# Performance work log

Measured on AMD Instinct MI355X. Metric: run time of the kernel, lower is better.

The kernel has to match this reference:

```python
import jax, jax.numpy as jnp
import numpy as np

INPUT_SIZE = 1024
HIDDEN = [2048, 2048]
OUTPUT_SIZE = 10
N = 16384
PRIOR_VAR = 100.0


def setup_inputs() -> dict:
    key = jax.random.key(0)
    ks = jax.random.split(key, 8)
    X = jax.random.normal(ks[0], (N, INPUT_SIZE), dtype=jnp.float32)
    Y = jax.random.randint(ks[1], (N,), 0, OUTPUT_SIZE, dtype=jnp.int32)
    # Kaiming-ish init like nn.Linear defaults (scale irrelevant to correctness)
    def lin(k, fan_in, fan_out):
        bound = 1.0 / np.sqrt(fan_in)
        kw, kb = jax.random.split(k)
        W = jax.random.uniform(kw, (fan_out, fan_in), jnp.float32, -bound, bound)
        b = jax.random.uniform(kb, (fan_out,), jnp.float32, -bound, bound)
        return W, b
    W1, b1 = lin(ks[2], INPUT_SIZE, HIDDEN[0])
    W2, b2 = lin(ks[3], HIDDEN[0], HIDDEN[1])
    W3, b3 = lin(ks[4], HIDDEN[1], OUTPUT_SIZE)
    return {"X": X, "Y": Y, "W1": W1, "b1": b1, "W2": W2, "b2": b2, "W3": W3, "b3": b3}


def reference(X, Y, W1, b1, W2, b2, W3, b3):
    # Batched version of the per-sample Linear+ReLU+...+Linear+Softmax(dim=0) loop.
    h = jax.nn.relu(X @ W1.T + b1)            # [N, H0]
    h = jax.nn.relu(h @ W2.T + b2)            # [N, H1]
    logits = h @ W3.T + b3                    # [N, C]
    # Categorical(probs=softmax(logits)).log_prob(Y[i]) == log_softmax(logits)[i, Y[i]]
    logp = jax.nn.log_softmax(logits, axis=-1)
    log_likelihood = jnp.sum(jnp.take_along_axis(logp, Y[:, None].astype(jnp.int32), axis=-1))
    # MVN(0, 100*I) log-prob over flattened params: closed-form diagonal Gaussian.
    params = (W1, b1, W2, b2, W3, b3)
    d = sum(p.size for p in params)
    sq = sum(jnp.sum(p * p) for p in params)
    log_prior = -0.5 * (sq / PRIOR_VAR + d * jnp.log(2.0 * jnp.pi * PRIOR_VAR))
    return log_likelihood + log_prior
```

## Files before the change

kernel.cpp:

```cpp
#include <hip/hip_runtime.h>
#include <math.h>

typedef __bf16 bf16;
typedef bf16 bf16x8 __attribute__((ext_vector_type(8)));
typedef bf16 bf16x4 __attribute__((ext_vector_type(4)));
typedef float f32x4 __attribute__((ext_vector_type(4)));

#define NROWS 16384
#define HID 2048

__global__ __launch_bounds__(256) void cvt_kernel(const float* __restrict__ src,
                                                  bf16* __restrict__ dst, int n4) {
  int stride = gridDim.x * blockDim.x;
  for (int i = blockIdx.x * blockDim.x + threadIdx.x; i < n4; i += stride) {
    float4 v = ((const float4*)src)[i];
    bf16x4 o;
    o[0] = (bf16)v.x; o[1] = (bf16)v.y; o[2] = (bf16)v.z; o[3] = (bf16)v.w;
    ((bf16x4*)dst)[i] = o;
  }
}

__device__ __forceinline__ void gload_lds16(const bf16* g, bf16* l) {
  __builtin_amdgcn_global_load_lds((const __attribute__((address_space(1))) void*)g,
                                   (__attribute__((address_space(3))) void*)l,
                                   16, 0, 0);
}

template <int K, bool RELU>
__global__ __launch_bounds__(512) void gemm256(const bf16* __restrict__ A,
                                               const bf16* __restrict__ B,
                                               const float* __restrict__ bias,
                                               bf16* __restrict__ C, int N) {
  extern __shared__ bf16 smem[];
  constexpr int NT = K / 32;
  const int tid = threadIdx.x;
  const int lane = tid & 63;
  const int w = tid >> 6;
  const int wr = w >> 2, wc = w & 3;

  const int c = blockIdx.x & 7, l = blockIdx.x >> 3;
  const int bm = c * 8 + (l >> 3);
  const int bn = l & 7;

  const bf16* Abase = A + (size_t)bm * 256 * K;
  const bf16* Bbase = B + (size_t)bn * 256 * K;

  const int r0 = tid >> 2;
  const int r1 = r0 + 128;
  const int kp = tid & 3;
  const size_t offS0 = (size_t)r0 * K + ((kp ^ ((r0 >> 1) & 3)) * 8);
  const size_t offS1 = (size_t)r1 * K + ((kp ^ ((r1 >> 1) & 3)) * 8);

  int offRA[8], offRB[4];
  const int kk = lane >> 4;
#pragma unroll
  for (int mi = 0; mi < 8; ++mi) {
    const int r = wr * 128 + mi * 16 + (lane & 15);
    offRA[mi] = (r * 4 + (kk ^ ((r >> 1) & 3))) * 8;
  }
#pragma unroll
  for (int ni = 0; ni < 4; ++ni) {
    const int r = wc * 64 + ni * 16 + (lane & 15);
    offRB[ni] = (r * 4 + (kk ^ ((r >> 1) & 3))) * 8 + 8192;
  }

  f32x4 acc[8][4] = {};

#define STAGE(t, b)                                                   \
  {                                                                   \
    const bf16* As = Abase + (size_t)(t) * 32;                        \
    const bf16* Bs = Bbase + (size_t)(t) * 32;                        \
    bf16* d = smem + (b) * 16384 + w * 512;    \
    gload_lds16(As + offS0, d);                                       \
    gload_lds16(As + offS1, d + 4096);                                \
    gload_lds16(Bs + offS0, d + 8192);                                \
    gload_lds16(Bs + offS1, d + 12288);                               \
  }

  STAGE(0, 0); STAGE(1, 1); STAGE(2, 2);
  asm volatile("s_waitcnt vmcnt(8)" ::: "memory");
  __builtin_amdgcn_s_barrier();
  asm volatile("" ::: "memory");

  for (int t = 0; t < NT; ++t) {
    if (t + 3 < NT) STAGE(t + 3, (t + 3) & 3);

    const bf16* base = smem + (t & 3) * 16384;
    bf16x8 af[8], bfr[4];
#pragma unroll
    for (int mi = 0; mi < 8; ++mi) af[mi] = *(const bf16x8*)(base + offRA[mi]);
#pragma unroll
    for (int ni = 0; ni < 4; ++ni) bfr[ni] = *(const bf16x8*)(base + offRB[ni]);

    __builtin_amdgcn_s_setprio(1);
#pragma unroll
    for (int mi = 0; mi < 8; ++mi)
#pragma unroll
      for (int ni = 0; ni < 4; ++ni)
        acc[mi][ni] = __builtin_amdgcn_mfma_f32_16x16x32_bf16(af[mi], bfr[ni], acc[mi][ni], 0, 0, 0);
    __builtin_amdgcn_s_setprio(0);
    asm volatile("" ::: "memory");

    if (t + 1 < NT) {
      if (t + 3 < NT)      asm volatile("s_waitcnt vmcnt(8)" ::: "memory");
      else if (t + 2 < NT) asm volatile("s_waitcnt vmcnt(4)" ::: "memory");
      else                 asm volatile("s_waitcnt vmcnt(0)" ::: "memory");
      __builtin_amdgcn_s_barrier();
      asm volatile("" ::: "memory");
    }
  }
#undef STAGE

  const int crow0 = bm * 256 + wr * 128 + (lane >> 4) * 4;
  const int ccol0 = bn * 256 + wc * 64 + (lane & 15);
#pragma unroll
  for (int mi = 0; mi < 8; ++mi) {
#pragma unroll
    for (int ni = 0; ni < 4; ++ni) {
      const int col = ccol0 + ni * 16;
      const float bv = bias[col];
#pragma unroll
      for (int j = 0; j < 4; ++j) {
        const int row = crow0 + mi * 16 + j;
        float v = acc[mi][ni][j] + bv;
        if (RELU) v = fmaxf(v, 0.f);
        C[(size_t)row * N + col] = (bf16)v;
      }
    }
  }
}

__global__ __launch_bounds__(256) void loss_kernel(const bf16* __restrict__ h2,
                                                   const bf16* __restrict__ W3b,
                                                   const float* __restrict__ b3,
                                                   const int* __restrict__ Y,
                                                   float* __restrict__ acc) {
  __shared__ bf16 w3s[10 * HID];
  for (int i = threadIdx.x; i < 10 * HID / 8; i += 256)
    ((bf16x8*)w3s)[i] = ((const bf16x8*)W3b)[i];
  __syncthreads();

  const int lane = threadIdx.x & 63;
  const int w = threadIdx.x >> 6;
  const int nwave = gridDim.x * 4;
  float lsum = 0.f;

  for (int row = blockIdx.x * 4 + w; row < NROWS; row += nwave) {
    float p[10];
#pragma unroll
    for (int c = 0; c < 10; ++c) p[c] = 0.f;
    const bf16* hrow = h2 + (size_t)row * HID;
#pragma unroll
    for (int it = 0; it < 4; ++it) {
      const int k = it * 512 + lane * 8;
      bf16x8 hv = *(const bf16x8*)&hrow[k];
      float hf[8];
#pragma unroll
      for (int j = 0; j < 8; ++j) hf[j] = (float)hv[j];
#pragma unroll
      for (int c = 0; c < 10; ++c) {
        bf16x8 wv = *(const bf16x8*)&w3s[c * HID + k];
        float dp = 0.f;
#pragma unroll
        for (int j = 0; j < 8; ++j) dp += hf[j] * (float)wv[j];
        p[c] += dp;
      }
    }
#pragma unroll
    for (int off = 32; off; off >>= 1)
#pragma unroll
      for (int c = 0; c < 10; ++c) p[c] += __shfl_xor(p[c], off, 64);

    float lg[10], m = -1e30f;
#pragma unroll
    for (int c = 0; c < 10; ++c) { lg[c] = p[c] + b3[c]; m = fmaxf(m, lg[c]); }
    float s = 0.f;
#pragma unroll
    for (int c = 0; c < 10; ++c) s += expf(lg[c] - m);
    const float lse = m + logf(s);
    const int y = Y[row];
    float ly = 0.f;
#pragma unroll
    for (int c = 0; c < 10; ++c) ly += (c == y) ? lg[c] : 0.f;
    lsum += ly - lse;
  }
  if (lane == 0) atomicAdd(&acc[0], lsum);
}

struct SqArgs { const float* p[6]; int n[6]; };

__global__ __launch_bounds__(256) void sumsq_kernel(SqArgs args, float* __restrict__ acc) {
  float s = 0.f;
  const int stride = gridDim.x * blockDim.x;
  for (int a = 0; a < 6; ++a) {
    const float* p = args.p[a];
    const int n = args.n[a];
    for (int i = blockIdx.x * blockDim.x + threadIdx.x; i < n; i += stride) {
      float v = p[i];
      s += v * v;
    }
  }
#pragma unroll
  for (int off = 32; off; off >>= 1) s += __shfl_xor(s, off, 64);
  if ((threadIdx.x & 63) == 0) atomicAdd(&acc[1], s);
}

__global__ void finalize_kernel(float* __restrict__ out, const float* __restrict__ acc,
                                double dterm) {
  out[0] = (float)((double)acc[0] - 0.5 * ((double)acc[1] / 100.0 + dterm));
}

extern "C" void kernel_launch(void* const* d_in, const int* in_sizes, int n_in,
                              void* d_out, int out_size, void* d_ws, size_t ws_size,
                              hipStream_t stream) {
  const float* X  = (const float*)d_in[0];
  const int*   Y  = (const int*)d_in[1];
  const float* W1 = (const float*)d_in[2];
  const float* b1 = (const float*)d_in[3];
  const float* W2 = (const float*)d_in[4];
  const float* b2 = (const float*)d_in[5];
  const float* W3 = (const float*)d_in[6];
  const float* b3 = (const float*)d_in[7];
  float* out = (float*)d_out;

  char* ws = (char*)d_ws;
  size_t off = 0;
  auto alloc = [&](size_t bytes) -> void* {
    void* p = ws + off;
    off += (bytes + 255) & ~(size_t)255;
    return p;
  };
  bf16* Xb  = (bf16*)alloc((size_t)NROWS * 1024 * 2);
  bf16* W1b = (bf16*)alloc((size_t)HID * 1024 * 2);
  bf16* W2b = (bf16*)alloc((size_t)HID * HID * 2);
  bf16* W3b = (bf16*)alloc((size_t)10 * HID * 2);
  bf16* h1  = (bf16*)alloc((size_t)NROWS * HID * 2);
  bf16* h2  = (bf16*)alloc((size_t)NROWS * HID * 2);
  float* acc = (float*)alloc(256);

  hipMemsetAsync(acc, 0, 16, stream);

  auto cvt = [&](const float* s, bf16* d, int n) {
    int n4 = n / 4;
    int grid = (n4 + 255) / 256;
    if (grid > 4096) grid = 4096;
    cvt_kernel<<<grid, 256, 0, stream>>>(s, d, n4);
  };
  cvt(X,  Xb,  NROWS * 1024);
  cvt(W1, W1b, HID * 1024);
  cvt(W2, W2b, HID * HID);
  cvt(W3, W3b, 10 * HID);

  SqArgs sq;
  sq.p[0] = W1; sq.n[0] = in_sizes[2];
  sq.p[1] = b1; sq.n[1] = in_sizes[3];
  sq.p[2] = W2; sq.n[2] = in_sizes[4];
  sq.p[3] = b2; sq.n[3] = in_sizes[5];
  sq.p[4] = W3; sq.n[4] = in_sizes[6];
  sq.p[5] = b3; sq.n[5] = in_sizes[7];
  sumsq_kernel<<<512, 256, 0, stream>>>(sq, acc);

  hipFuncSetAttribute((const void*)gemm256<1024, true>,
                      hipFuncAttributeMaxDynamicSharedMemorySize, 131072);
  hipFuncSetAttribute((const void*)gemm256<2048, true>,
                      hipFuncAttributeMaxDynamicSharedMemorySize, 131072);

  gemm256<1024, true><<<512, 512, 131072, stream>>>(Xb, W1b, b1, h1, HID);
  gemm256<2048, true><<<512, 512, 131072, stream>>>(h1, W2b, b2, h2, HID);

  loss_kernel<<<256, 256, 0, stream>>>(h2, W3b, b3, Y, acc);

  long long d = 0;
  for (int i = 2; i < 8; ++i) d += in_sizes[i];
  double dterm = (double)d * log(2.0 * M_PI * 100.0);
  finalize_kernel<<<1, 1, 0, stream>>>(out, acc, dterm);
}
```

Measured before the change: 436.7 us.

## Restructure GEMM to 64-wide K double-buffer pipeline and fuse conversion with sum-of-squares

The GEMM now loads 64-wide K tiles into two 64KB LDS buffers with an 8-slot XOR swizzle. Global-to-LDS staging of the next tile is interleaved in half-tile pieces between MFMA groups, separated by barriers. The four conversion kernels and the sumsq kernel are merged into one pass that converts to bf16 and accumulates squares, with b3 squares moved into finalize. The loss kernel grid grows from 256 to 1024 blocks. The many extra barriers per tile and the launch_bounds(512,2) register cap may cost throughput or cause spills.

```diff
diff --git a/kernel.cpp b/kernel.cpp
--- a/kernel.cpp
+++ b/kernel.cpp
@@ -9,107 +9,145 @@
 #define NROWS 16384
 #define HID 2048
 
-__global__ __launch_bounds__(256) void cvt_kernel(const float* __restrict__ src,
-                                                  bf16* __restrict__ dst, int n4) {
-  int stride = gridDim.x * blockDim.x;
-  for (int i = blockIdx.x * blockDim.x + threadIdx.x; i < n4; i += stride) {
-    float4 v = ((const float4*)src)[i];
-    bf16x4 o;
-    o[0] = (bf16)v.x; o[1] = (bf16)v.y; o[2] = (bf16)v.z; o[3] = (bf16)v.w;
-    ((bf16x4*)dst)[i] = o;
-  }
-}
-
 __device__ __forceinline__ void gload_lds16(const bf16* g, bf16* l) {
   __builtin_amdgcn_global_load_lds((const __attribute__((address_space(1))) void*)g,
                                    (__attribute__((address_space(3))) void*)l,
                                    16, 0, 0);
 }
 
+#define MF(a, b, c) __builtin_amdgcn_mfma_f32_16x16x32_bf16((a), (b), (c), 0, 0, 0)
+
+#define BAR()                                  \
+  asm volatile("" ::: "memory");               \
+  __builtin_amdgcn_s_barrier();                \
+  asm volatile("" ::: "memory");
+
 template <int K, bool RELU>
-__global__ __launch_bounds__(512) void gemm256(const bf16* __restrict__ A,
-                                               const bf16* __restrict__ B,
-                                               const float* __restrict__ bias,
-                                               bf16* __restrict__ C, int N) {
+__global__ __launch_bounds__(512, 2) void gemm256(const bf16* __restrict__ A,
+                                                  const bf16* __restrict__ B,
+                                                  const float* __restrict__ bias,
+                                                  bf16* __restrict__ C, int N) {
   extern __shared__ bf16 smem[];
-  constexpr int NT = K / 32;
+  constexpr int NT = K / 64;
+  constexpr int NI = NT / 2;
   const int tid = threadIdx.x;
   const int lane = tid & 63;
   const int w = tid >> 6;
   const int wr = w >> 2, wc = w & 3;
 
-  const int c = blockIdx.x & 7, l = blockIdx.x >> 3;
-  const int bm = c * 8 + (l >> 3);
-  const int bn = l & 7;
+  const int xc = blockIdx.x & 7, xl = blockIdx.x >> 3;
+  const int bm = xc * 8 + (xl >> 3);
+  const int bn = xl & 7;
 
   const bf16* Abase = A + (size_t)bm * 256 * K;
   const bf16* Bbase = B + (size_t)bn * 256 * K;
 
-  const int r0 = tid >> 2;
-  const int r1 = r0 + 128;
-  const int kp = tid & 3;
-  const size_t offS0 = (size_t)r0 * K + ((kp ^ ((r0 >> 1) & 3)) * 8);
-  const size_t offS1 = (size_t)r1 * K + ((kp ^ ((r1 >> 1) & 3)) * 8);
-
-  int offRA[8], offRB[4];
-  const int kk = lane >> 4;
-#pragma unroll
-  for (int mi = 0; mi < 8; ++mi) {
-    const int r = wr * 128 + mi * 16 + (lane & 15);
-    offRA[mi] = (r * 4 + (kk ^ ((r >> 1) & 3))) * 8;
-  }
-#pragma unroll
-  for (int ni = 0; ni < 4; ++ni) {
-    const int r = wc * 64 + ni * 16 + (lane & 15);
-    offRB[ni] = (r * 4 + (kk ^ ((r >> 1) & 3))) * 8 + 8192;
-  }
+  const int srow = tid >> 3;
+  const int sslot = (tid & 7) ^ (srow & 7);
+
+  const int q0 = (lane >> 4) ^ (lane & 7);
+  const int q1 = q0 ^ 4;
+  int rbA[8], rbB[4];
+#pragma unroll
+  for (int mi = 0; mi < 8; ++mi)
+    rbA[mi] = (wr * 128 + mi * 16 + (lane & 15)) * 64;
+#pragma unroll
+  for (int ni = 0; ni < 4; ++ni)
+    rbB[ni] = 16384 + (wc * 64 + ni * 16 + (lane & 15)) * 64;
 
   f32x4 acc[8][4] = {};
-
-#define STAGE(t, b)                                                   \
-  {                                                                   \
-    const bf16* As = Abase + (size_t)(t) * 32;                        \
-    const bf16* Bs = Bbase + (size_t)(t) * 32;                        \
-    bf16* d = smem + (b) * 16384 + w * 512;    \
-    gload_lds16(As + offS0, d);                                       \
-    gload_lds16(As + offS1, d + 4096);                                \
-    gload_lds16(Bs + offS0, d + 8192);                                \
-    gload_lds16(Bs + offS1, d + 12288);                               \
-  }
-
-  STAGE(0, 0); STAGE(1, 1); STAGE(2, 2);
-  asm volatile("s_waitcnt vmcnt(8)" ::: "memory");
-  __builtin_amdgcn_s_barrier();
-  asm volatile("" ::: "memory");
-
-  for (int t = 0; t < NT; ++t) {
-    if (t + 3 < NT) STAGE(t + 3, (t + 3) & 3);
-
-    const bf16* base = smem + (t & 3) * 16384;
-    bf16x8 af[8], bfr[4];
-#pragma unroll
-    for (int mi = 0; mi < 8; ++mi) af[mi] = *(const bf16x8*)(base + offRA[mi]);
-#pragma unroll
-    for (int ni = 0; ni < 4; ++ni) bfr[ni] = *(const bf16x8*)(base + offRB[ni]);
-
-    __builtin_amdgcn_s_setprio(1);
-#pragma unroll
-    for (int mi = 0; mi < 8; ++mi)
-#pragma unroll
-      for (int ni = 0; ni < 4; ++ni)
-        acc[mi][ni] = __builtin_amdgcn_mfma_f32_16x16x32_bf16(af[mi], bfr[ni], acc[mi][ni], 0, 0, 0);
-    __builtin_amdgcn_s_setprio(0);
-    asm volatile("" ::: "memory");
-
-    if (t + 1 < NT) {
-      if (t + 3 < NT)      asm volatile("s_waitcnt vmcnt(8)" ::: "memory");
-      else if (t + 2 < NT) asm volatile("s_waitcnt vmcnt(4)" ::: "memory");
-      else                 asm volatile("s_waitcnt vmcnt(0)" ::: "memory");
-      __builtin_amdgcn_s_barrier();
-      asm volatile("" ::: "memory");
+  bf16x8 av[4], bv[4];
+
+#define LD8(off) (*(const bf16x8*)(smem + (off)))
+
+#define READS_A(bb, qk, mh)                                  \
+  av[0] = LD8((bb)*32768 + rbA[(mh)*4 + 0] + (qk)*8);        \
+  av[1] = LD8((bb)*32768 + rbA[(mh)*4 + 1] + (qk)*8);        \
+  av[2] = LD8((bb)*32768 + rbA[(mh)*4 + 2] + (qk)*8);        \
+  av[3] = LD8((bb)*32768 + rbA[(mh)*4 + 3] + (qk)*8);
+
+#define READS_B(bb, qk)                                      \
+  bv[0] = LD8((bb)*32768 + rbB[0] + (qk)*8);                 \
+  bv[1] = LD8((bb)*32768 + rbB[1] + (qk)*8);                 \
+  bv[2] = LD8((bb)*32768 + rbB[2] + (qk)*8);                 \
+  bv[3] = LD8((bb)*32768 + rbB[3] + (qk)*8);
+
+#define MFMA16(mh)                                           \
+  __builtin_amdgcn_s_setprio(1);                             \
+  acc[(mh)*4+0][0] = MF(av[0], bv[0], acc[(mh)*4+0][0]);     \
+  acc[(mh)*4+0][1] = MF(av[0], bv[1], acc[(mh)*4+0][1]);     \
+  acc[(mh)*4+0][2] = MF(av[0], bv[2], acc[(mh)*4+0][2]);     \
+  acc[(mh)*4+0][3] = MF(av[0], bv[3], acc[(mh)*4+0][3]);     \
+  acc[(mh)*4+1][0] = MF(av[1], bv[0], acc[(mh)*4+1][0]);     \
+  acc[(mh)*4+1][1] = MF(av[1], bv[1], acc[(mh)*4+1][1]);     \
+  acc[(mh)*4+1][2] = MF(av[1], bv[2], acc[(mh)*4+1][2]);     \
+  acc[(mh)*4+1][3] = MF(av[1], bv[3], acc[(mh)*4+1][3]);     \
+  acc[(mh)*4+2][0] = MF(av[2], bv[0], acc[(mh)*4+2][0]);     \
+  acc[(mh)*4+2][1] = MF(av[2], bv[1], acc[(mh)*4+2][1]);     \
+  acc[(mh)*4+2][2] = MF(av[2], bv[2], acc[(mh)*4+2][2]);     \
+  acc[(mh)*4+2][3] = MF(av[2], bv[3], acc[(mh)*4+2][3]);     \
+  acc[(mh)*4+3][0] = MF(av[3], bv[0], acc[(mh)*4+3][0]);     \
+  acc[(mh)*4+3][1] = MF(av[3], bv[1], acc[(mh)*4+3][1]);     \
+  acc[(mh)*4+3][2] = MF(av[3], bv[2], acc[(mh)*4+3][2]);     \
+  acc[(mh)*4+3][3] = MF(av[3], bv[3], acc[(mh)*4+3][3]);     \
+  __builtin_amdgcn_s_setprio(0);
+
+#define STAGE_HALF(isB, h, t, bb)                                                  \
+  {                                                                                \
+    const bf16* gs = ((isB) ? Bbase : Abase) + (size_t)((h)*128) * K + (t) * 64;   \
+    bf16* ld = smem + (bb)*32768 + (isB)*16384 + (h)*8192 + w * 512;               \
+    gload_lds16(gs + (size_t)srow * K + sslot * 8, ld);                            \
+    gload_lds16(gs + (size_t)(srow + 64) * K + sslot * 8, ld + 4096);              \
+  }
+
+  STAGE_HALF(0, 0, 0, 0); STAGE_HALF(0, 1, 0, 0);
+  STAGE_HALF(1, 0, 0, 0); STAGE_HALF(1, 1, 0, 0);
+
+  for (int it = 0; it < NI; ++it) {
+    const int T = 2 * it;
+    const bool s47 = (it < NI - 1);
+
+    STAGE_HALF(0, 0, T + 1, 1);
+    asm volatile("s_waitcnt vmcnt(2)" ::: "memory");
+    BAR();
+    READS_B(0, q0); READS_A(0, q0, 0);
+    MFMA16(0);
+    BAR();
+    READS_A(0, q0, 1);
+    STAGE_HALF(0, 1, T + 1, 1);
+    MFMA16(1);
+    BAR();
+    READS_B(0, q1); READS_A(0, q1, 0);
+    STAGE_HALF(1, 0, T + 1, 1);
+    MFMA16(0);
+    BAR();
+    READS_A(0, q1, 1);
+    STAGE_HALF(1, 1, T + 1, 1);
+    MFMA16(1);
+    BAR();
+    if (s47) {
+      STAGE_HALF(0, 0, T + 2, 0);
+      asm volatile("s_waitcnt vmcnt(2)" ::: "memory");
+    } else {
+      asm volatile("s_waitcnt vmcnt(0)" ::: "memory");
     }
-  }
-#undef STAGE
+    BAR();
+    READS_B(1, q0); READS_A(1, q0, 0);
+    MFMA16(0);
+    BAR();
+    READS_A(1, q0, 1);
+    if (s47) STAGE_HALF(0, 1, T + 2, 0);
+    MFMA16(1);
+    BAR();
+    READS_B(1, q1); READS_A(1, q1, 0);
+    if (s47) STAGE_HALF(1, 0, T + 2, 0);
+    MFMA16(0);
+    BAR();
+    READS_A(1, q1, 1);
+    if (s47) STAGE_HALF(1, 1, T + 2, 0);
+    MFMA16(1);
+    BAR();
+  }
 
   const int crow0 = bm * 256 + wr * 128 + (lane >> 4) * 4;
   const int ccol0 = bn * 256 + wc * 64 + (lane & 15);
@@ -118,16 +156,47 @@
 #pragma unroll
     for (int ni = 0; ni < 4; ++ni) {
       const int col = ccol0 + ni * 16;
-      const float bv = bias[col];
+      const float bvv = bias[col];
 #pragma unroll
       for (int j = 0; j < 4; ++j) {
         const int row = crow0 + mi * 16 + j;
-        float v = acc[mi][ni][j] + bv;
+        float v = acc[mi][ni][j] + bvv;
         if (RELU) v = fmaxf(v, 0.f);
         C[(size_t)row * N + col] = (bf16)v;
       }
     }
   }
+}
+
+struct CvtSqArgs {
+  const float* src[6];
+  bf16* dst[6];
+  int n4[6];
+  int dosq[6];
+};
+
+__global__ __launch_bounds__(256) void cvtsq_kernel(CvtSqArgs a, float* __restrict__ acc) {
+  float s = 0.f;
+  const int stride = gridDim.x * blockDim.x;
+#pragma unroll 1
+  for (int seg = 0; seg < 6; ++seg) {
+    const float4* src = (const float4*)a.src[seg];
+    bf16x4* dst = (bf16x4*)a.dst[seg];
+    const int n4 = a.n4[seg];
+    const bool dq = a.dosq[seg] != 0;
+    for (int i = blockIdx.x * blockDim.x + threadIdx.x; i < n4; i += stride) {
+      float4 v = src[i];
+      if (dst) {
+        bf16x4 o;
+        o[0] = (bf16)v.x; o[1] = (bf16)v.y; o[2] = (bf16)v.z; o[3] = (bf16)v.w;
+        dst[i] = o;
+      }
+      if (dq) s += v.x * v.x + v.y * v.y + v.z * v.z + v.w * v.w;
+    }
+  }
+#pragma unroll
+  for (int off = 32; off; off >>= 1) s += __shfl_xor(s, off, 64);
+  if ((threadIdx.x & 63) == 0) atomicAdd(&acc[1], s);
 }
 
 __global__ __launch_bounds__(256) void loss_kernel(const bf16* __restrict__ h2,
@@ -187,27 +256,11 @@
   if (lane == 0) atomicAdd(&acc[0], lsum);
 }
 
-struct SqArgs { const float* p[6]; int n[6]; };
-
-__global__ __launch_bounds__(256) void sumsq_kernel(SqArgs args, float* __restrict__ acc) {
-  float s = 0.f;
-  const int stride = gridDim.x * blockDim.x;
-  for (int a = 0; a < 6; ++a) {
-    const float* p = args.p[a];
-    const int n = args.n[a];
-    for (int i = blockIdx.x * blockDim.x + threadIdx.x; i < n; i += stride) {
-      float v = p[i];
-      s += v * v;
-    }
-  }
-#pragma unroll
-  for (int off = 32; off; off >>= 1) s += __shfl_xor(s, off, 64);
-  if ((threadIdx.x & 63) == 0) atomicAdd(&acc[1], s);
-}
-
 __global__ void finalize_kernel(float* __restrict__ out, const float* __restrict__ acc,
-                                double dterm) {
-  out[0] = (float)((double)acc[0] - 0.5 * ((double)acc[1] / 100.0 + dterm));
+                                const float* __restrict__ b3, double dterm) {
+  double sq = (double)acc[1];
+  for (int i = 0; i < 10; ++i) sq += (double)b3[i] * (double)b3[i];
+  out[0] = (float)((double)acc[0] - 0.5 * (sq / 100.0 + dterm));
 }
 
 extern "C" void kernel_launch(void* const* d_in, const int* in_sizes, int n_in,
@@ -240,25 +293,14 @@
 
   hipMemsetAsync(acc, 0, 16, stream);
 
-  auto cvt = [&](const float* s, bf16* d, int n) {
-    int n4 = n / 4;
-    int grid = (n4 + 255) / 256;
-    if (grid > 4096) grid = 4096;
-    cvt_kernel<<<grid, 256, 0, stream>>>(s, d, n4);
-  };
-  cvt(X,  Xb,  NROWS * 1024);
-  cvt(W1, W1b, HID * 1024);
-  cvt(W2, W2b, HID * HID);
-  cvt(W3, W3b, 10 * HID);
-
-  SqArgs sq;
-  sq.p[0] = W1; sq.n[0] = in_sizes[2];
-  sq.p[1] = b1; sq.n[1] = in_sizes[3];
-  sq.p[2] = W2; sq.n[2] = in_sizes[4];
-  sq.p[3] = b2; sq.n[3] = in_sizes[5];
-  sq.p[4] = W3; sq.n[4] = in_sizes[6];
-  sq.p[5] = b3; sq.n[5] = in_sizes[7];
-  sumsq_kernel<<<512, 256, 0, stream>>>(sq, acc);
+  CvtSqArgs ca;
+  ca.src[0] = X;  ca.dst[0] = Xb;  ca.n4[0] = NROWS * 1024 / 4; ca.dosq[0] = 0;
+  ca.src[1] = W1; ca.dst[1] = W1b; ca.n4[1] = HID * 1024 / 4;   ca.dosq[1] = 1;
+  ca.src[2] = W2; ca.dst[2] = W2b; ca.n4[2] = HID * HID / 4;    ca.dosq[2] = 1;
+  ca.src[3] = W3; ca.dst[3] = W3b; ca.n4[3] = 10 * HID / 4;     ca.dosq[3] = 1;
+  ca.src[4] = b1; ca.dst[4] = nullptr; ca.n4[4] = HID / 4;      ca.dosq[4] = 1;
+  ca.src[5] = b2; ca.dst[5] = nullptr; ca.n4[5] = HID / 4;      ca.dosq[5] = 1;
+  cvtsq_kernel<<<2048, 256, 0, stream>>>(ca, acc);
 
   hipFuncSetAttribute((const void*)gemm256<1024, true>,
                       hipFuncAttributeMaxDynamicSharedMemorySize, 131072);
@@ -268,10 +310,10 @@
   gemm256<1024, true><<<512, 512, 131072, stream>>>(Xb, W1b, b1, h1, HID);
   gemm256<2048, true><<<512, 512, 131072, stream>>>(h1, W2b, b2, h2, HID);
 
-  loss_kernel<<<256, 256, 0, stream>>>(h2, W3b, b3, Y, acc);
+  loss_kernel<<<1024, 256, 0, stream>>>(h2, W3b, b3, Y, acc);
 
   long long d = 0;
   for (int i = 2; i < 8; ++i) d += in_sizes[i];
   double dterm = (double)d * log(2.0 * M_PI * 100.0);
-  finalize_kernel<<<1, 1, 0, stream>>>(out, acc, dterm);
-}
+  finalize_kernel<<<1, 1, 0, stream>>>(out, acc, b3, dterm);
+}
```

Result: slower. 493.5 us (+13.0%).

## Software-pipeline GEMM LDS fragment loads, fuse convert with sum-of-squares, widen loss grid

Applied to the files above, without the earlier changes.

The GEMM inner loop now processes two K-tiles per iteration and splits A fragments into halves. The next half's LDS reads are issued while the current 16 MFMAs run, so shared-memory latency overlaps with matrix math. The kernel also gets a two-block-per-CU launch bound hint. The four conversion kernels and the sum-of-squares kernel are merged into one pass that reads each weight once, with the b3 squares moved to finalize. The loss kernel grid grows from 256 to 1024 blocks. Together these add register pressure and more complex wait-count logic.

```diff
diff --git a/kernel.cpp b/kernel.cpp
--- a/kernel.cpp
+++ b/kernel.cpp
@@ -9,28 +9,28 @@
 #define NROWS 16384
 #define HID 2048
 
-__global__ __launch_bounds__(256) void cvt_kernel(const float* __restrict__ src,
-                                                  bf16* __restrict__ dst, int n4) {
-  int stride = gridDim.x * blockDim.x;
-  for (int i = blockIdx.x * blockDim.x + threadIdx.x; i < n4; i += stride) {
-    float4 v = ((const float4*)src)[i];
-    bf16x4 o;
-    o[0] = (bf16)v.x; o[1] = (bf16)v.y; o[2] = (bf16)v.z; o[3] = (bf16)v.w;
-    ((bf16x4*)dst)[i] = o;
-  }
-}
-
 __device__ __forceinline__ void gload_lds16(const bf16* g, bf16* l) {
   __builtin_amdgcn_global_load_lds((const __attribute__((address_space(1))) void*)g,
                                    (__attribute__((address_space(3))) void*)l,
                                    16, 0, 0);
 }
 
+#define MF(a, b, c) __builtin_amdgcn_mfma_f32_16x16x32_bf16((a), (b), (c), 0, 0, 0)
+
+#define BAR()                                  \
+  asm volatile("" ::: "memory");               \
+  __builtin_amdgcn_s_barrier();                \
+  asm volatile("" ::: "memory");
+
+#define LGKM0()                                           \
+  asm volatile("s_waitcnt lgkmcnt(0)" ::: "memory");      \
+  __builtin_amdgcn_sched_barrier(0);
+
 template <int K, bool RELU>
-__global__ __launch_bounds__(512) void gemm256(const bf16* __restrict__ A,
-                                               const bf16* __restrict__ B,
-                                               const float* __restrict__ bias,
-                                               bf16* __restrict__ C, int N) {
+__global__ __launch_bounds__(512, 2) void gemm256(const bf16* __restrict__ A,
+                                                  const bf16* __restrict__ B,
+                                                  const float* __restrict__ bias,
+                                                  bf16* __restrict__ C, int N) {
   extern __shared__ bf16 smem[];
   constexpr int NT = K / 32;
   const int tid = threadIdx.x;
@@ -38,9 +38,9 @@
   const int w = tid >> 6;
   const int wr = w >> 2, wc = w & 3;
 
-  const int c = blockIdx.x & 7, l = blockIdx.x >> 3;
-  const int bm = c * 8 + (l >> 3);
-  const int bn = l & 7;
+  const int xc = blockIdx.x & 7, xl = blockIdx.x >> 3;
+  const int bm = xc * 8 + (xl >> 3);
+  const int bn = xl & 7;
 
   const bf16* Abase = A + (size_t)bm * 256 * K;
   const bf16* Bbase = B + (size_t)bn * 256 * K;
@@ -65,6 +65,9 @@
   }
 
   f32x4 acc[8][4] = {};
+  bf16x8 a0[4], a1[4], b0[4], b1[4];
+
+#define LD8(off) (*(const bf16x8*)(smem + (off)))
 
 #define STAGE(t, b)                                                   \
   {                                                                   \
@@ -77,39 +80,79 @@
     gload_lds16(Bs + offS1, d + 12288);                               \
   }
 
+#define MFMA16(AV, BV, mh)                                           \
+  __builtin_amdgcn_s_setprio(1);                                     \
+  acc[(mh)*4+0][0] = MF(AV[0], BV[0], acc[(mh)*4+0][0]);             \
+  acc[(mh)*4+0][1] = MF(AV[0], BV[1], acc[(mh)*4+0][1]);             \
+  acc[(mh)*4+0][2] = MF(AV[0], BV[2], acc[(mh)*4+0][2]);             \
+  acc[(mh)*4+0][3] = MF(AV[0], BV[3], acc[(mh)*4+0][3]);             \
+  acc[(mh)*4+1][0] = MF(AV[1], BV[0], acc[(mh)*4+1][0]);             \
+  acc[(mh)*4+1][1] = MF(AV[1], BV[1], acc[(mh)*4+1][1]);             \
+  acc[(mh)*4+1][2] = MF(AV[1], BV[2], acc[(mh)*4+1][2]);             \
+  acc[(mh)*4+1][3] = MF(AV[1], BV[3], acc[(mh)*4+1][3]);             \
+  acc[(mh)*4+2][0] = MF(AV[2], BV[0], acc[(mh)*4+2][0]);             \
+  acc[(mh)*4+2][1] = MF(AV[2], BV[1], acc[(mh)*4+2][1]);             \
+  acc[(mh)*4+2][2] = MF(AV[2], BV[2], acc[(mh)*4+2][2]);             \
+  acc[(mh)*4+2][3] = MF(AV[2], BV[3], acc[(mh)*4+2][3]);             \
+  acc[(mh)*4+3][0] = MF(AV[3], BV[0], acc[(mh)*4+3][0]);             \
+  acc[(mh)*4+3][1] = MF(AV[3], BV[1], acc[(mh)*4+3][1]);             \
+  acc[(mh)*4+3][2] = MF(AV[3], BV[2], acc[(mh)*4+3][2]);             \
+  acc[(mh)*4+3][3] = MF(AV[3], BV[3], acc[(mh)*4+3][3]);             \
+  __builtin_amdgcn_s_setprio(0);
+
   STAGE(0, 0); STAGE(1, 1); STAGE(2, 2);
   asm volatile("s_waitcnt vmcnt(8)" ::: "memory");
-  __builtin_amdgcn_s_barrier();
-  asm volatile("" ::: "memory");
-
-  for (int t = 0; t < NT; ++t) {
+  BAR();
+  {
+#pragma unroll
+    for (int i = 0; i < 4; ++i) b0[i] = LD8(offRB[i]);
+#pragma unroll
+    for (int i = 0; i < 4; ++i) a0[i] = LD8(offRA[i]);
+  }
+
+  for (int t = 0; t < NT; t += 2) {
     if (t + 3 < NT) STAGE(t + 3, (t + 3) & 3);
-
-    const bf16* base = smem + (t & 3) * 16384;
-    bf16x8 af[8], bfr[4];
-#pragma unroll
-    for (int mi = 0; mi < 8; ++mi) af[mi] = *(const bf16x8*)(base + offRA[mi]);
-#pragma unroll
-    for (int ni = 0; ni < 4; ++ni) bfr[ni] = *(const bf16x8*)(base + offRB[ni]);
-
-    __builtin_amdgcn_s_setprio(1);
-#pragma unroll
-    for (int mi = 0; mi < 8; ++mi)
-#pragma unroll
-      for (int ni = 0; ni < 4; ++ni)
-        acc[mi][ni] = __builtin_amdgcn_mfma_f32_16x16x32_bf16(af[mi], bfr[ni], acc[mi][ni], 0, 0, 0);
-    __builtin_amdgcn_s_setprio(0);
-    asm volatile("" ::: "memory");
-
-    if (t + 1 < NT) {
-      if (t + 3 < NT)      asm volatile("s_waitcnt vmcnt(8)" ::: "memory");
-      else if (t + 2 < NT) asm volatile("s_waitcnt vmcnt(4)" ::: "memory");
-      else                 asm volatile("s_waitcnt vmcnt(0)" ::: "memory");
-      __builtin_amdgcn_s_barrier();
-      asm volatile("" ::: "memory");
-    }
-  }
-#undef STAGE
+    {
+      const int bb = (t & 3) * 16384;
+#pragma unroll
+      for (int i = 0; i < 4; ++i) a1[i] = LD8(bb + offRA[4 + i]);
+    }
+    MFMA16(a0, b0, 0);
+    LGKM0();
+    if (t + 3 < NT)      asm volatile("s_waitcnt vmcnt(8)" ::: "memory");
+    else if (t + 2 < NT) asm volatile("s_waitcnt vmcnt(4)" ::: "memory");
+    else                 asm volatile("s_waitcnt vmcnt(0)" ::: "memory");
+    BAR();
+    {
+      const int nb = ((t + 1) & 3) * 16384;
+#pragma unroll
+      for (int i = 0; i < 4; ++i) b1[i] = LD8(nb + offRB[i]);
+#pragma unroll
+      for (int i = 0; i < 4; ++i) a0[i] = LD8(nb + offRA[i]);
+    }
+    MFMA16(a1, b0, 1);
+
+    if (t + 4 < NT) STAGE(t + 4, (t + 4) & 3);
+    {
+      const int bb = ((t + 1) & 3) * 16384;
+#pragma unroll
+      for (int i = 0; i < 4; ++i) a1[i] = LD8(bb + offRA[4 + i]);
+    }
+    MFMA16(a0, b1, 0);
+    LGKM0();
+    if (t + 4 < NT)      asm volatile("s_waitcnt vmcnt(8)" ::: "memory");
+    else if (t + 3 < NT) asm volatile("s_waitcnt vmcnt(4)" ::: "memory");
+    else                 asm volatile("s_waitcnt vmcnt(0)" ::: "memory");
+    if (t + 2 < NT) {
+      BAR();
+      const int nb = ((t + 2) & 3) * 16384;
+#pragma unroll
+      for (int i = 0; i < 4; ++i) b0[i] = LD8(nb + offRB[i]);
+#pragma unroll
+      for (int i = 0; i < 4; ++i) a0[i] = LD8(nb + offRA[i]);
+    }
+    MFMA16(a1, b1, 1);
+  }
 
   const int crow0 = bm * 256 + wr * 128 + (lane >> 4) * 4;
   const int ccol0 = bn * 256 + wc * 64 + (lane & 15);
@@ -118,16 +161,69 @@
 #pragma unroll
     for (int ni = 0; ni < 4; ++ni) {
       const int col = ccol0 + ni * 16;
-      const float bv = bias[col];
+      const float bvv = bias[col];
 #pragma unroll
       for (int j = 0; j < 4; ++j) {
         const int row = crow0 + mi * 16 + j;
-        float v = acc[mi][ni][j] + bv;
+        float v = acc[mi][ni][j] + bvv;
         if (RELU) v = fmaxf(v, 0.f);
         C[(size_t)row * N + col] = (bf16)v;
       }
     }
   }
+}
+
+struct CvtSqArgs {
+  const float* src[6];
+  bf16* dst[6];
+  int n4[6];
+  int dosq[6];
+};
+
+__global__ __launch_bounds__(256) void cvtsq_kernel(CvtSqArgs a, float* __restrict__ acc) {
+  float s = 0.f;
+  const int S = gridDim.x * blockDim.x;
+  const int gid = blockIdx.x * blockDim.x + threadIdx.x;
+#pragma unroll 1
+  for (int seg = 0; seg < 6; ++seg) {
+    const float4* __restrict__ src = (const float4*)a.src[seg];
+    bf16x4* __restrict__ dst = (bf16x4*)a.dst[seg];
+    const int n4 = a.n4[seg];
+    const bool dq = a.dosq[seg] != 0;
+    const int nb = n4 & ~(4 * S - 1);
+    for (int i = gid; i < nb; i += 4 * S) {
+      float4 v0 = src[i];
+      float4 v1 = src[i + S];
+      float4 v2 = src[i + 2 * S];
+      float4 v3 = src[i + 3 * S];
+      if (dst) {
+        bf16x4 o0, o1, o2, o3;
+        o0[0]=(bf16)v0.x; o0[1]=(bf16)v0.y; o0[2]=(bf16)v0.z; o0[3]=(bf16)v0.w;
+        o1[0]=(bf16)v1.x; o1[1]=(bf16)v1.y; o1[2]=(bf16)v1.z; o1[3]=(bf16)v1.w;
+        o2[0]=(bf16)v2.x; o2[1]=(bf16)v2.y; o2[2]=(bf16)v2.z; o2[3]=(bf16)v2.w;
+        o3[0]=(bf16)v3.x; o3[1]=(bf16)v3.y; o3[2]=(bf16)v3.z; o3[3]=(bf16)v3.w;
+        dst[i] = o0; dst[i + S] = o1; dst[i + 2 * S] = o2; dst[i + 3 * S] = o3;
+      }
+      if (dq) {
+        s += v0.x*v0.x + v0.y*v0.y + v0.z*v0.z + v0.w*v0.w;
+        s += v1.x*v1.x + v1.y*v1.y + v1.z*v1.z + v1.w*v1.w;
+        s += v2.x*v2.x + v2.y*v2.y + v2.z*v2.z + v2.w*v2.w;
+        s += v3.x*v3.x + v3.y*v3.y + v3.z*v3.z + v3.w*v3.w;
+      }
+    }
+    for (int i = nb + gid; i < n4; i += S) {
+      float4 v = src[i];
+      if (dst) {
+        bf16x4 o;
+        o[0]=(bf16)v.x; o[1]=(bf16)v.y; o[2]=(bf16)v.z; o[3]=(bf16)v.w;
+        dst[i] = o;
+      }
+      if (dq) s += v.x*v.x + v.y*v.y + v.z*v.z + v.w*v.w;
+    }
+  }
+#pragma unroll
+  for (int off = 32; off; off >>= 1) s += __shfl_xor(s, off, 64);
+  if ((threadIdx.x & 63) == 0) atomicAdd(&acc[1], s);
 }
 
 __global__ __launch_bounds__(256) void loss_kernel(const bf16* __restrict__ h2,
@@ -187,27 +283,11 @@
   if (lane == 0) atomicAdd(&acc[0], lsum);
 }
 
-struct SqArgs { const float* p[6]; int n[6]; };
-
-__global__ __launch_bounds__(256) void sumsq_kernel(SqArgs args, float* __restrict__ acc) {
-  float s = 0.f;
-  const int stride = gridDim.x * blockDim.x;
-  for (int a = 0; a < 6; ++a) {
-    const float* p = args.p[a];
-    const int n = args.n[a];
-    for (int i = blockIdx.x * blockDim.x + threadIdx.x; i < n; i += stride) {
-      float v = p[i];
-      s += v * v;
-    }
-  }
-#pragma unroll
-  for (int off = 32; off; off >>= 1) s += __shfl_xor(s, off, 64);
-  if ((threadIdx.x & 63) == 0) atomicAdd(&acc[1], s);
-}
-
 __global__ void finalize_kernel(float* __restrict__ out, const float* __restrict__ acc,
-                                double dterm) {
-  out[0] = (float)((double)acc[0] - 0.5 * ((double)acc[1] / 100.0 + dterm));
+                                const float* __restrict__ b3, double dterm) {
+  double sq = (double)acc[1];
+  for (int i = 0; i < 10; ++i) sq += (double)b3[i] * (double)b3[i];
+  out[0] = (float)((double)acc[0] - 0.5 * (sq / 100.0 + dterm));
 }
 
 extern "C" void kernel_launch(void* const* d_in, const int* in_sizes, int n_in,
@@ -240,25 +320,14 @@
 
   hipMemsetAsync(acc, 0, 16, stream);
 
-  auto cvt = [&](const float* s, bf16* d, int n) {
-    int n4 = n / 4;
-    int grid = (n4 + 255) / 256;
-    if (grid > 4096) grid = 4096;
-    cvt_kernel<<<grid, 256, 0, stream>>>(s, d, n4);
-  };
-  cvt(X,  Xb,  NROWS * 1024);
-  cvt(W1, W1b, HID * 1024);
-  cvt(W2, W2b, HID * HID);
-  cvt(W3, W3b, 10 * HID);
-
-  SqArgs sq;
-  sq.p[0] = W1; sq.n[0] = in_sizes[2];
-  sq.p[1] = b1; sq.n[1] = in_sizes[3];
-  sq.p[2] = W2; sq.n[2] = in_sizes[4];
-  sq.p[3] = b2; sq.n[3] = in_sizes[5];
-  sq.p[4] = W3; sq.n[4] = in_sizes[6];
-  sq.p[5] = b3; sq.n[5] = in_sizes[7];
-  sumsq_kernel<<<512, 256, 0, stream>>>(sq, acc);
+  CvtSqArgs ca;
+  ca.src[0] = X;  ca.dst[0] = Xb;  ca.n4[0] = NROWS * 1024 / 4; ca.dosq[0] = 0;
+  ca.src[1] = W1; ca.dst[1] = W1b; ca.n4[1] = HID * 1024 / 4;   ca.dosq[1] = 1;
+  ca.src[2] = W2; ca.dst[2] = W2b; ca.n4[2] = HID * HID / 4;    ca.dosq[2] = 1;
+  ca.src[3] = W3; ca.dst[3] = W3b; ca.n4[3] = 10 * HID / 4;     ca.dosq[3] = 1;
+  ca.src[4] = b1; ca.dst[4] = nullptr; ca.n4[4] = HID / 4;      ca.dosq[4] = 1;
+  ca.src[5] = b2; ca.dst[5] = nullptr; ca.n4[5] = HID / 4;      ca.dosq[5] = 1;
+  cvtsq_kernel<<<512, 256, 0, stream>>>(ca, acc);
 
   hipFuncSetAttribute((const void*)gemm256<1024, true>,
                       hipFuncAttributeMaxDynamicSharedMemorySize, 131072);
@@ -268,10 +337,10 @@
   gemm256<1024, true><<<512, 512, 131072, stream>>>(Xb, W1b, b1, h1, HID);
   gemm256<2048, true><<<512, 512, 131072, stream>>>(h1, W2b, b2, h2, HID);
 
-  loss_kernel<<<256, 256, 0, stream>>>(h2, W3b, b3, Y, acc);
+  loss_kernel<<<1024, 256, 0, stream>>>(h2, W3b, b3, Y, acc);
 
   long long d = 0;
   for (int i = 2; i < 8; ++i) d += in_sizes[i];
   double dterm = (double)d * log(2.0 * M_PI * 100.0);
-  finalize_kernel<<<1, 1, 0, stream>>>(out, acc, dterm);
-}
+  finalize_kernel<<<1, 1, 0, stream>>>(out, acc, b3, dterm);
+}
```

Result: faster. 416.5 us (-4.6%).
